# Kernel optimization log

Hardware: AMD Instinct MI355X
Metric: run time of the kernel (lower is better)

Reference implementation:

```python
import jax, jax.numpy as jnp
import numpy as np
import math

# e3nn-style fully-connected Clebsch-Gordan tensor product
# irreps_in1 = 64x0e + 64x1e + 64x2e   (dim 576)
# irreps_in2 =  1x0e +  1x1e +  1x2e   (dim 9, e.g. spherical harmonics)
# irreps_out = 64x0e + 64x1e + 64x2e   (dim 576), shared weights
MUL1, MUL2, MULO = 64, 1, 64
LS = [0, 1, 2]
N_BATCH = 32768


def _su2_cg(j1, m1, j2, m2, j3, m3):
    # SU(2) Clebsch-Gordan coefficient <j1 m1 j2 m2 | j3 m3> (Racah formula)
    if m3 != m1 + m2:
        return 0.0
    f = math.factorial
    c = (2 * j3 + 1) * f(j1 + j2 - j3) * f(j1 - j2 + j3) * f(-j1 + j2 + j3) / f(j1 + j2 + j3 + 1)
    c = math.sqrt(c)
    c *= math.sqrt(f(j3 + m3) * f(j3 - m3) * f(j1 - m1) * f(j1 + m1) * f(j2 - m2) * f(j2 + m2))
    s = 0.0
    for k in range(max(0, j2 - j3 - m1, j1 - j3 + m2), min(j1 + j2 - j3, j1 - m1, j2 + m2) + 1):
        s += (-1.0) ** k / (f(k) * f(j1 + j2 - j3 - k) * f(j1 - m1 - k) * f(j2 + m2 - k)
                            * f(j3 - j2 + m1 + k) * f(j3 - j1 - m2 + k))
    return c * s


def _q_real_to_complex(l):
    # unitary change of basis, columns = real-SH index, rows = complex m (e3nn convention)
    q = np.zeros((2 * l + 1, 2 * l + 1), dtype=np.complex128)
    r2 = 1.0 / math.sqrt(2.0)
    for m in range(-l, 0):
        q[l + m, l + abs(m)] = r2
        q[l + m, l - abs(m)] = -1j * r2
    q[l, l] = 1.0
    for m in range(1, l + 1):
        q[l + m, l + m] = (-1) ** m * r2
        q[l + m, l - m] = 1j * (-1) ** m * r2
    return (-1j) ** l * q


def _real_cg(l1, l2, l3):
    # CG tensor in the real spherical-harmonic basis, unit Frobenius norm (wigner_3j-like)
    C = np.zeros((2 * l1 + 1, 2 * l2 + 1, 2 * l3 + 1), dtype=np.complex128)
    for m1 in range(-l1, l1 + 1):
        for m2 in range(-l2, l2 + 1):
            m3 = m1 + m2
            if abs(m3) <= l3:
                C[l1 + m1, l2 + m2, l3 + m3] = _su2_cg(l1, m1, l2, m2, l3, m3)
    U1, U2, U3 = _q_real_to_complex(l1), _q_real_to_complex(l2), _q_real_to_complex(l3)
    Cr = np.einsum('ia,jb,kc,ijk->abc', U1, U2, np.conj(U3), C)
    assert np.abs(Cr.imag).max() < 1e-9, 'real-basis CG should be real'
    Cr = Cr.real
    return (Cr / np.linalg.norm(Cr)).astype(np.float32)


PATHS = [(l1, l2, l3) for l1 in LS for l2 in LS for l3 in LS if abs(l1 - l2) <= l3 <= l1 + l2]
CG = {p: jnp.asarray(_real_cg(*p)) for p in PATHS}
N_PATHS_TO = {l3: sum(1 for p in PATHS if p[2] == l3) for l3 in LS}
ALPHA = {l3: 1.0 / math.sqrt(MUL1 * MUL2 * N_PATHS_TO[l3]) for l3 in LS}  # path normalization
WEIGHT_NUMEL = len(PATHS) * MUL1 * MUL2 * MULO  # 15 * 4096 = 61440
DIM1 = MUL1 * sum(2 * l + 1 for l in LS)  # 576
DIM2 = MUL2 * sum(2 * l + 1 for l in LS)  # 9


def _split1(x):
    segs, off = [], 0
    for l in LS:
        d = MUL1 * (2 * l + 1)
        segs.append(x[:, off:off + d].reshape(-1, MUL1, 2 * l + 1))
        off += d
    return segs


def _split2(y):
    segs, off = [], 0
    for l in LS:
        d = 2 * l + 1
        segs.append(y[:, off:off + d])
        off += d
    return segs


def tensor_product(x, y, W):
    # W (x (CG-otimes) y): per-path weighted Clebsch-Gordan contraction
    xs, ys = _split1(x), _split2(y)  # xs[l]: [N,64,2l+1], ys[l]: [N,2l+1]
    N = x.shape[0]
    outs = [jnp.zeros((N, MULO, 2 * l + 1), x.dtype) for l in LS]
    off = 0
    for (l1, l2, l3) in PATHS:
        Wp = W[off:off + MUL1 * MULO].reshape(MUL1, MULO)  # [u, w] (v = 1)
        off += MUL1 * MULO
        outs[l3] = outs[l3] + ALPHA[l3] * jnp.einsum(
            'nui,nj,ijk,uw->nwk', xs[l1], ys[l2], CG[(l1, l2, l3)], Wp)
    return jnp.concatenate([o.reshape(N, -1) for o in outs], axis=-1)  # [N, 576]


def setup_inputs() -> dict:
    key = jax.random.key(0)
    kx, ky, kw = jax.random.split(key, 3)
    x = jax.random.normal(kx, (N_BATCH, DIM1), dtype=jnp.float32)
    y = jax.random.normal(ky, (N_BATCH, DIM2), dtype=jnp.float32)
    W = jax.random.normal(kw, (WEIGHT_NUMEL,), dtype=jnp.float32)
    return {'x': x, 'y': y, 'W': W}


def reference(x, y, W):
    return tensor_product(x, y, W)
```

## Files before the change

kernel.cpp:

```cpp
#include <hip/hip_runtime.h>
#include <cmath>
#include <complex>
#include <algorithm>

#define NPATH 15
constexpr int PL1[NPATH] = {0,0,0, 1,1,1,1,1,1, 2,2,2,2,2,2};
constexpr int PL2[NPATH] = {0,1,2, 0,1,1,1,2,2, 0,1,1,2,2,2};
constexpr int PL3[NPATH] = {0,1,2, 1,0,1,2,1,2, 2,1,2,0,1,2};
constexpr int CGOFF[NPATH] = {0,1,10,35,44,53,80,125,170,245,270,315,390,415,490};
constexpr int CGTOT = 615;
constexpr int YOFF[3] = {0,1,4};

constexpr int GB[8] = {0,9,24,33,48,63,88,103};
constexpr int YGTOT = 137;

struct CGArg { float v[CGTOT]; };

static double factd(int n){ double r=1.0; for(int i=2;i<=n;++i) r*=(double)i; return r; }

static double su2_cg(int j1,int m1,int j2,int m2,int j3,int m3){
  if (m3 != m1+m2) return 0.0;
  double c = (double)(2*j3+1) * factd(j1+j2-j3) * factd(j1-j2+j3) * factd(-j1+j2+j3)
             / factd(j1+j2+j3+1);
  c = std::sqrt(c);
  c *= std::sqrt(factd(j3+m3)*factd(j3-m3)*factd(j1-m1)*factd(j1+m1)*factd(j2-m2)*factd(j2+m2));
  double s = 0.0;
  int kmin = std::max(0, std::max(j2-j3-m1, j1-j3+m2));
  int kmax = std::min(j1+j2-j3, std::min(j1-m1, j2+m2));
  for (int k=kmin;k<=kmax;++k){
    double d = factd(k)*factd(j1+j2-j3-k)*factd(j1-m1-k)*factd(j2+m2-k)
             * factd(j3-j2+m1+k)*factd(j3-j1-m2+k);
    s += ((k&1)? -1.0 : 1.0)/d;
  }
  return c*s;
}

static void qmat(int l, std::complex<double>* q){
  int d = 2*l+1;
  for (int a=0;a<d*d;++a) q[a] = std::complex<double>(0.0,0.0);
  const double r2 = 1.0/std::sqrt(2.0);
  for (int m=-l; m<0; ++m){
    q[(l+m)*d + (l-m)] = std::complex<double>(r2, 0.0);
    q[(l+m)*d + (l+m)] = std::complex<double>(0.0, -r2);
  }
  q[l*d + l] = std::complex<double>(1.0,0.0);
  for (int m=1; m<=l; ++m){
    double sg = (m&1)? -1.0 : 1.0;
    q[(l+m)*d + (l+m)] = std::complex<double>(sg*r2, 0.0);
    q[(l+m)*d + (l-m)] = std::complex<double>(0.0, sg*r2);
  }
  std::complex<double> ph = (l==0)? std::complex<double>(1,0)
                        : (l==1)? std::complex<double>(0,-1)
                                : std::complex<double>(-1,0);
  for (int a=0;a<d*d;++a) q[a] *= ph;
}

static void compute_cg(float* outv){
  const int npaths_to[3] = {3,6,6};
  for (int p=0;p<NPATH;++p){
    int l1=PL1[p], l2=PL2[p], l3=PL3[p];
    int d1=2*l1+1, d2=2*l2+1, d3=2*l3+1;
    std::complex<double> C[5][5][5];
    for (int a=0;a<5;++a) for(int b=0;b<5;++b) for(int c=0;c<5;++c) C[a][b][c]=std::complex<double>(0,0);
    for (int m1=-l1;m1<=l1;++m1) for (int m2=-l2;m2<=l2;++m2){
      int m3=m1+m2;
      if (std::abs(m3)<=l3) C[l1+m1][l2+m2][l3+m3] = su2_cg(l1,m1,l2,m2,l3,m3);
    }
    std::complex<double> U1[25],U2[25],U3[25];
    qmat(l1,U1); qmat(l2,U2); qmat(l3,U3);
    double Cr[5][5][5]; double nrm=0.0;
    for (int a=0;a<d1;++a) for (int b=0;b<d2;++b) for (int c=0;c<d3;++c){
      std::complex<double> s(0,0);
      for (int i=0;i<d1;++i) for (int j=0;j<d2;++j) for (int k=0;k<d3;++k)
        s += U1[i*d1+a]*U2[j*d2+b]*std::conj(U3[k*d3+c])*C[i][j][k];
      Cr[a][b][c] = s.real();
      nrm += s.real()*s.real();
    }
    nrm = std::sqrt(nrm);
    double alpha = 1.0/std::sqrt(64.0*(double)npaths_to[l3]);
    float* o = outv + CGOFF[p];
    int idx=0;
    for (int a=0;a<d1;++a) for (int b=0;b<d2;++b) for (int c=0;c<d3;++c)
      o[idx++] = (float)(Cr[a][b][c]/nrm*alpha);
  }
}

typedef short bf16x8 __attribute__((ext_vector_type(8)));
typedef float f32x4 __attribute__((ext_vector_type(4)));

#define MFMA16(A,B,C) __builtin_amdgcn_mfma_f32_16x16x32_bf16((A),(B),(C),0,0,0)

__device__ __forceinline__ unsigned cvtpk_bf16(float a, float b){
  unsigned r;
  asm("v_cvt_pk_bf16_f32 %0, %1, %2" : "=v"(r) : "v"(a), "v"(b));
  return r;
}

__device__ __forceinline__ bf16x8 afrag(const unsigned short* s_xt, int plane, int kt, int row, int q){
  int c = (kt*4 + q) ^ (row & 7);
  return *reinterpret_cast<const bf16x8*>(s_xt + (plane*16 + row)*64 + c*8);
}
__device__ __forceinline__ bf16x8 wfrag(const unsigned short* WT, int p, int wt, int cl, int kt, int q){
  return *reinterpret_cast<const bf16x8*>(WT + p*4096 + (wt*16+cl)*64 + kt*32 + q*8);
}
__device__ __forceinline__ void xt_write_pk(unsigned short* s_xt, int plane, int n, int t16, uint2 pk){
  const int swz = (((t16>>1)^(n&7))<<3) + ((t16&1)<<2);
  *reinterpret_cast<uint2*>(s_xt + (plane*16 + n)*64 + swz) = pk;
}

__device__ __forceinline__ void pack_x(const float4& r0, const float4* r1, const float4* r2, uint2* xpk){
  const float* f0 = reinterpret_cast<const float*>(&r0);
  const float* f1 = reinterpret_cast<const float*>(r1);
  const float* f2 = reinterpret_cast<const float*>(r2);
  xpk[0].x = cvtpk_bf16(f0[0], f0[1]);  xpk[0].y = cvtpk_bf16(f0[2], f0[3]);
  #pragma unroll
  for (int i=0;i<3;++i){
    xpk[1+i].x = cvtpk_bf16(f1[0*3+i], f1[1*3+i]);
    xpk[1+i].y = cvtpk_bf16(f1[2*3+i], f1[3*3+i]);
  }
  #pragma unroll
  for (int i=0;i<5;++i){
    xpk[4+i].x = cvtpk_bf16(f2[0*5+i], f2[1*5+i]);
    xpk[4+i].y = cvtpk_bf16(f2[2*5+i], f2[3*5+i]);
  }
}

template<int G,int PB,int D1,int D3,int AB>
__device__ __forceinline__ void gen1(const unsigned short* s_xt, bf16x8 b0, bf16x8 b1,
                                     const float* yg4, f32x4* acc, int cl, int q){
  const f32x4 z4 = {0.f,0.f,0.f,0.f};
  #pragma unroll
  for (int i=0;i<D1;++i){
    bf16x8 a0 = afrag(s_xt, PB+i, 0, cl, q);
    bf16x8 a1 = afrag(s_xt, PB+i, 1, cl, q);
    f32x4 T = MFMA16(a0, b0, z4);  T = MFMA16(a1, b1, T);
    #pragma unroll
    for (int k=0;k<D3;++k){
      f32x4 yv = *reinterpret_cast<const f32x4*>(yg4 + (GB[G] + i*D3 + k)*16);
      acc[AB+k] += T*yv;
    }
  }
}
template<int PB,int D1,int AB>
__device__ __forceinline__ void dl0(const unsigned short* s_xt, bf16x8 b0, bf16x8 b1,
                                    f32x4 cy, f32x4* acc, int cl, int q){
  const f32x4 z4 = {0.f,0.f,0.f,0.f};
  #pragma unroll
  for (int i=0;i<D1;++i){
    bf16x8 a0 = afrag(s_xt, PB+i, 0, cl, q);
    bf16x8 a1 = afrag(s_xt, PB+i, 1, cl, q);
    f32x4 T = MFMA16(a0, b0, z4);  T = MFMA16(a1, b1, T);
    acc[AB+i] += cy*T;
  }
}
template<int D3,int YE,int AB>
__device__ __forceinline__ void d0l(const unsigned short* s_xt, bf16x8 b0, bf16x8 b1,
                                    float c, const float* yg4, f32x4* acc, int cl, int q){
  const f32x4 z4 = {0.f,0.f,0.f,0.f};
  bf16x8 a0 = afrag(s_xt, 0, 0, cl, q);
  bf16x8 a1 = afrag(s_xt, 0, 1, cl, q);
  f32x4 T = MFMA16(a0, b0, z4);  T = MFMA16(a1, b1, T);
  #pragma unroll
  for (int k=0;k<D3;++k){
    f32x4 yv = *reinterpret_cast<const f32x4*>(yg4 + (YE+k)*16);
    acc[AB+k] += (c*yv)*T;
  }
}
template<int PB,int D1,int YE>
__device__ __forceinline__ void dll0(const unsigned short* s_xt, bf16x8 b0, bf16x8 b1,
                                     float c, const float* yg4, f32x4* acc, int cl, int q){
  const f32x4 z4 = {0.f,0.f,0.f,0.f};
  f32x4 s = z4;
  #pragma unroll
  for (int i=0;i<D1;++i){
    bf16x8 a0 = afrag(s_xt, PB+i, 0, cl, q);
    bf16x8 a1 = afrag(s_xt, PB+i, 1, cl, q);
    f32x4 T = MFMA16(a0, b0, z4);  T = MFMA16(a1, b1, T);
    f32x4 yv = *reinterpret_cast<const f32x4*>(yg4 + (YE+i)*16);
    s += yv*T;
  }
  acc[0] += s*c;
}

__global__ __launch_bounds__(256, 4)
void tp_kernel(const float* __restrict__ x, const float* __restrict__ y,
               const unsigned short* __restrict__ WT, float* __restrict__ out, CGArg cga)
{
  __shared__ __align__(16) unsigned short s_xt[9*16*64];
  __shared__ __align__(16) float s_yg[YGTOT*16];

  const int bid = blockIdx.x;
  const int tile = (bid & 7) | ((bid >> 4) << 3);
  const int half = (bid >> 3) & 1;
  const int n0 = tile * 16;

  const int tid = threadIdx.x;
  const int n_s = tid>>4, t16 = tid&15;

  {
    const float* xb = x + (size_t)(n0 + n_s)*576;
    float4 r0 = *reinterpret_cast<const float4*>(xb + t16*4);
    float4 r1[3], r2[5];
    #pragma unroll
    for (int i=0;i<3;++i) r1[i] = *reinterpret_cast<const float4*>(xb + 64 + t16*12 + 4*i);
    #pragma unroll
    for (int i=0;i<5;++i) r2[i] = *reinterpret_cast<const float4*>(xb + 256 + t16*20 + 4*i);

    float yl[9];
    {
      const float* yrow = y + (size_t)(n0 + t16)*9;
      #pragma unroll
      for (int j=0;j<9;++j) yl[j] = yrow[j];
    }

    uint2 xpk[9];
    pack_x(r0, r1, r2, xpk);
    #pragma unroll
    for (int pl=0; pl<9; ++pl) xt_write_pk(s_xt, pl, n_s, t16, xpk[pl]);

    if (tid < 16){
      #pragma unroll
      for (int j=0;j<9;++j) s_yg[(128+j)*16 + tid] = yl[j];
    }

    if (half == 0){
      constexpr int GL[4] = {0,2,4,6};
      #pragma unroll
      for (int u=0; u<4; ++u){
        constexpr int GPp[4] = {5,7,10,13};
        const int p = GPp[u];
        const int d2=2*PL2[p]+1, d3=2*PL3[p]+1;
        const int cnt = (2*PL1[p]+1)*d3*16;
        for (int idx=tid; idx<cnt; idx+=256){
          int ik = idx >> 4;
          int i  = ik/d3;
          int k  = ik - i*d3;
          float s=0.f;
          for (int j=0;j<d2;++j)
            s += yl[YOFF[PL2[p]]+j]*cga.v[CGOFF[p]+(i*d2+j)*d3+k];
          s_yg[(GB[GL[u]]+ik)*16 + t16] = s;
        }
      }
    } else {
      constexpr int GL[4] = {1,3,5,7};
      #pragma unroll
      for (int u=0; u<4; ++u){
        constexpr int GPp[4] = {6,8,11,14};
        const int p = GPp[u];
        const int d2=2*PL2[p]+1, d3=2*PL3[p]+1;
        const int cnt = (2*PL1[p]+1)*d3*16;
        for (int idx=tid; idx<cnt; idx+=256){
          int ik = idx >> 4;
          int i  = ik/d3;
          int k  = ik - i*d3;
          float s=0.f;
          for (int j=0;j<d2;++j)
            s += yl[YOFF[PL2[p]]+j]*cga.v[CGOFF[p]+(i*d2+j)*d3+k];
          s_yg[(GB[GL[u]]+ik)*16 + t16] = s;
        }
      }
    }
  }
  __syncthreads();

  const int lane = tid & 63, wt = tid >> 6;
  const int cl = lane & 15, q = lane >> 4;
  const float* yg4 = s_yg + q*4;
  #define YV(E) (*reinterpret_cast<const f32x4*>(yg4 + (E)*16))

  const f32x4 z4 = {0.f,0.f,0.f,0.f};
  bf16x8 b0,b1,nb0,nb1;
  const f32x4 y0v = YV(128);
  const int wc = wt*16 + cl;

  #define LDB(P) { nb0 = wfrag(WT,P,wt,cl,0,q); nb1 = wfrag(WT,P,wt,cl,1,q); }
  #define ADV    { b0 = nb0; b1 = nb1; }

  if (half == 0){
    f32x4 acc[4] = {z4,z4,z4,z4};
    b0 = wfrag(WT,0,wt,cl,0,q); b1 = wfrag(WT,0,wt,cl,1,q);
    LDB(1);  dl0<0,1,0>(s_xt,b0,b1, cga.v[CGOFF[0]]*y0v, acc, cl,q);            ADV;
    LDB(3);  d0l<3,129,1>(s_xt,b0,b1, cga.v[CGOFF[1]], yg4, acc, cl,q);         ADV;
    LDB(4);  dl0<1,3,1>(s_xt,b0,b1, cga.v[CGOFF[3]]*y0v, acc, cl,q);            ADV;
    LDB(5);  dll0<1,3,129>(s_xt,b0,b1, cga.v[CGOFF[4]], yg4, acc, cl,q);        ADV;
    LDB(7);  gen1<0,1,3,3,1>(s_xt,b0,b1, yg4, acc, cl,q);                       ADV;
    LDB(10); gen1<2,1,3,3,1>(s_xt,b0,b1, yg4, acc, cl,q);                       ADV;
    LDB(12); gen1<4,4,5,3,1>(s_xt,b0,b1, yg4, acc, cl,q);                       ADV;
    LDB(13); dll0<4,5,132>(s_xt,b0,b1, cga.v[CGOFF[12]], yg4, acc, cl,q);       ADV;
             gen1<6,4,5,3,1>(s_xt,b0,b1, yg4, acc, cl,q);
    #pragma unroll
    for (int r=0;r<4;++r){
      float* orow = out + (size_t)(n0 + q*4 + r)*576;
      orow[wc] = acc[0][r];
      #pragma unroll
      for (int k=0;k<3;++k) orow[64 + wc*3 + k] = acc[1+k][r];
    }
  } else {
    f32x4 acc[5] = {z4,z4,z4,z4,z4};
    b0 = wfrag(WT,2,wt,cl,0,q); b1 = wfrag(WT,2,wt,cl,1,q);
    LDB(6);  d0l<5,132,0>(s_xt,b0,b1, cga.v[CGOFF[2]], yg4, acc, cl,q);         ADV;
    LDB(8);  gen1<1,1,3,5,0>(s_xt,b0,b1, yg4, acc, cl,q);                       ADV;
    LDB(9);  gen1<3,1,3,5,0>(s_xt,b0,b1, yg4, acc, cl,q);                       ADV;
    LDB(11); dl0<4,5,0>(s_xt,b0,b1, cga.v[CGOFF[9]]*y0v, acc, cl,q);            ADV;
    LDB(14); gen1<5,4,5,5,0>(s_xt,b0,b1, yg4, acc, cl,q);                       ADV;
             gen1<7,4,5,5,0>(s_xt,b0,b1, yg4, acc, cl,q);
    #pragma unroll
    for (int r=0;r<4;++r){
      float* orow = out + (size_t)(n0 + q*4 + r)*576;
      #pragma unroll
      for (int k=0;k<5;++k) orow[256 + wc*5 + k] = acc[k][r];
    }
  }
  #undef LDB
  #undef ADV
  #undef YV
}

__global__ void wt_kernel(const float* __restrict__ W, unsigned short* __restrict__ WT){
  int t = blockIdx.x*256 + threadIdx.x;
  int p = t >> 12, r = t & 4095, w = r >> 6, u = r & 63;
  float f = W[(p<<12) + (u<<6) + w];
  unsigned fu = __builtin_bit_cast(unsigned, f);
  unsigned rr = (fu + 0x7FFFu + ((fu>>16)&1u)) >> 16;
  WT[t] = (unsigned short)rr;
}

extern "C" void kernel_launch(void* const* d_in, const int* in_sizes, int n_in,
                              void* d_out, int out_size, void* d_ws, size_t ws_size,
                              hipStream_t stream) {
  const float* x = (const float*)d_in[0];
  const float* y = (const float*)d_in[1];
  const float* W = (const float*)d_in[2];
  float* out = (float*)d_out;
  (void)in_sizes; (void)n_in; (void)out_size; (void)ws_size;

  unsigned short* WT = (unsigned short*)d_ws;

  CGArg cga;
  compute_cg(cga.v);

  hipLaunchKernelGGL(wt_kernel, dim3(240), dim3(256), 0, stream, W, WT);
  hipLaunchKernelGGL(tp_kernel, dim3(4096), dim3(256), 0, stream, x, y, WT, out, cga);
}
```

Baseline: 57.25 us.

## Swap MFMA operand roles to hoist x fragments and vectorize output stores

Swaps the A/B operands of the MFMA so the accumulator layout becomes row = batch lane, column = 4 consecutive output channels. This lets each lane write contiguous float4 chunks of the interleaved output instead of scalar strided stores. The x fragments for each l1 block are now loaded from shared memory once and reused across paths rather than reloaded per path. The y-CG scalars become per-lane scalars rather than f32x4 vectors. The held x fragments (up to 18 bf16x8 registers) raise register pressure, which could hurt occupancy under the 256x4 launch bounds.

```diff
diff --git a/kernel.cpp b/kernel.cpp
--- a/kernel.cpp
+++ b/kernel.cpp
@@ -125,59 +125,50 @@
   }
 }
 
-template<int G,int PB,int D1,int D3,int AB>
-__device__ __forceinline__ void gen1(const unsigned short* s_xt, bf16x8 b0, bf16x8 b1,
-                                     const float* yg4, f32x4* acc, int cl, int q){
+template<int G,int D1,int D3,int AB>
+__device__ __forceinline__ void gen1(const bf16x8* xf, bf16x8 b0, bf16x8 b1,
+                                     const float* ygc, f32x4* acc){
   const f32x4 z4 = {0.f,0.f,0.f,0.f};
   #pragma unroll
   for (int i=0;i<D1;++i){
-    bf16x8 a0 = afrag(s_xt, PB+i, 0, cl, q);
-    bf16x8 a1 = afrag(s_xt, PB+i, 1, cl, q);
-    f32x4 T = MFMA16(a0, b0, z4);  T = MFMA16(a1, b1, T);
+    f32x4 T = MFMA16(b0, xf[2*i], z4);  T = MFMA16(b1, xf[2*i+1], T);
     #pragma unroll
     for (int k=0;k<D3;++k){
-      f32x4 yv = *reinterpret_cast<const f32x4*>(yg4 + (GB[G] + i*D3 + k)*16);
+      float yv = ygc[(GB[G] + i*D3 + k)*16];
       acc[AB+k] += T*yv;
     }
   }
 }
-template<int PB,int D1,int AB>
-__device__ __forceinline__ void dl0(const unsigned short* s_xt, bf16x8 b0, bf16x8 b1,
-                                    f32x4 cy, f32x4* acc, int cl, int q){
+template<int D1,int AB>
+__device__ __forceinline__ void dl0(const bf16x8* xf, bf16x8 b0, bf16x8 b1,
+                                    float cy, f32x4* acc){
   const f32x4 z4 = {0.f,0.f,0.f,0.f};
   #pragma unroll
   for (int i=0;i<D1;++i){
-    bf16x8 a0 = afrag(s_xt, PB+i, 0, cl, q);
-    bf16x8 a1 = afrag(s_xt, PB+i, 1, cl, q);
-    f32x4 T = MFMA16(a0, b0, z4);  T = MFMA16(a1, b1, T);
-    acc[AB+i] += cy*T;
+    f32x4 T = MFMA16(b0, xf[2*i], z4);  T = MFMA16(b1, xf[2*i+1], T);
+    acc[AB+i] += T*cy;
   }
 }
 template<int D3,int YE,int AB>
-__device__ __forceinline__ void d0l(const unsigned short* s_xt, bf16x8 b0, bf16x8 b1,
-                                    float c, const float* yg4, f32x4* acc, int cl, int q){
-  const f32x4 z4 = {0.f,0.f,0.f,0.f};
-  bf16x8 a0 = afrag(s_xt, 0, 0, cl, q);
-  bf16x8 a1 = afrag(s_xt, 0, 1, cl, q);
-  f32x4 T = MFMA16(a0, b0, z4);  T = MFMA16(a1, b1, T);
+__device__ __forceinline__ void d0l(const bf16x8* xf, bf16x8 b0, bf16x8 b1,
+                                    float c, const float* ygc, f32x4* acc){
+  const f32x4 z4 = {0.f,0.f,0.f,0.f};
+  f32x4 T = MFMA16(b0, xf[0], z4);  T = MFMA16(b1, xf[1], T);
   #pragma unroll
   for (int k=0;k<D3;++k){
-    f32x4 yv = *reinterpret_cast<const f32x4*>(yg4 + (YE+k)*16);
-    acc[AB+k] += (c*yv)*T;
-  }
-}
-template<int PB,int D1,int YE>
-__device__ __forceinline__ void dll0(const unsigned short* s_xt, bf16x8 b0, bf16x8 b1,
-                                     float c, const float* yg4, f32x4* acc, int cl, int q){
+    float yv = c*ygc[(YE+k)*16];
+    acc[AB+k] += T*yv;
+  }
+}
+template<int D1,int YE>
+__device__ __forceinline__ void dll0(const bf16x8* xf, bf16x8 b0, bf16x8 b1,
+                                     float c, const float* ygc, f32x4* acc){
   const f32x4 z4 = {0.f,0.f,0.f,0.f};
   f32x4 s = z4;
   #pragma unroll
   for (int i=0;i<D1;++i){
-    bf16x8 a0 = afrag(s_xt, PB+i, 0, cl, q);
-    bf16x8 a1 = afrag(s_xt, PB+i, 1, cl, q);
-    f32x4 T = MFMA16(a0, b0, z4);  T = MFMA16(a1, b1, T);
-    f32x4 yv = *reinterpret_cast<const f32x4*>(yg4 + (YE+i)*16);
-    s += yv*T;
+    f32x4 T = MFMA16(b0, xf[2*i], z4);  T = MFMA16(b1, xf[2*i+1], T);
+    s += T*ygc[(YE+i)*16];
   }
   acc[0] += s*c;
 }
@@ -265,55 +256,86 @@
 
   const int lane = tid & 63, wt = tid >> 6;
   const int cl = lane & 15, q = lane >> 4;
-  const float* yg4 = s_yg + q*4;
-  #define YV(E) (*reinterpret_cast<const f32x4*>(yg4 + (E)*16))
+  const float* ygc = s_yg + cl;
+  const float y0 = ygc[128*16];
+  const int wbase = wt*16 + q*4;
 
   const f32x4 z4 = {0.f,0.f,0.f,0.f};
   bf16x8 b0,b1,nb0,nb1;
-  const f32x4 y0v = YV(128);
-  const int wc = wt*16 + cl;
 
   #define LDB(P) { nb0 = wfrag(WT,P,wt,cl,0,q); nb1 = wfrag(WT,P,wt,cl,1,q); }
   #define ADV    { b0 = nb0; b1 = nb1; }
 
   if (half == 0){
     f32x4 acc[4] = {z4,z4,z4,z4};
+    bf16x8 xf0[2];
+    #pragma unroll
+    for (int kt=0;kt<2;++kt) xf0[kt] = afrag(s_xt, 0, kt, cl, q);
     b0 = wfrag(WT,0,wt,cl,0,q); b1 = wfrag(WT,0,wt,cl,1,q);
-    LDB(1);  dl0<0,1,0>(s_xt,b0,b1, cga.v[CGOFF[0]]*y0v, acc, cl,q);            ADV;
-    LDB(3);  d0l<3,129,1>(s_xt,b0,b1, cga.v[CGOFF[1]], yg4, acc, cl,q);         ADV;
-    LDB(4);  dl0<1,3,1>(s_xt,b0,b1, cga.v[CGOFF[3]]*y0v, acc, cl,q);            ADV;
-    LDB(5);  dll0<1,3,129>(s_xt,b0,b1, cga.v[CGOFF[4]], yg4, acc, cl,q);        ADV;
-    LDB(7);  gen1<0,1,3,3,1>(s_xt,b0,b1, yg4, acc, cl,q);                       ADV;
-    LDB(10); gen1<2,1,3,3,1>(s_xt,b0,b1, yg4, acc, cl,q);                       ADV;
-    LDB(12); gen1<4,4,5,3,1>(s_xt,b0,b1, yg4, acc, cl,q);                       ADV;
-    LDB(13); dll0<4,5,132>(s_xt,b0,b1, cga.v[CGOFF[12]], yg4, acc, cl,q);       ADV;
-             gen1<6,4,5,3,1>(s_xt,b0,b1, yg4, acc, cl,q);
-    #pragma unroll
-    for (int r=0;r<4;++r){
-      float* orow = out + (size_t)(n0 + q*4 + r)*576;
-      orow[wc] = acc[0][r];
-      #pragma unroll
-      for (int k=0;k<3;++k) orow[64 + wc*3 + k] = acc[1+k][r];
-    }
+
+    LDB(1);  dl0<1,0>(xf0, b0,b1, cga.v[CGOFF[0]]*y0, acc);              ADV;
+    LDB(3);  d0l<3,129,1>(xf0, b0,b1, cga.v[CGOFF[1]], ygc, acc);        ADV;
+    bf16x8 xf1[6];
+    #pragma unroll
+    for (int i=0;i<3;++i)
+      #pragma unroll
+      for (int kt=0;kt<2;++kt) xf1[2*i+kt] = afrag(s_xt, 1+i, kt, cl, q);
+    LDB(4);  dl0<3,1>(xf1, b0,b1, cga.v[CGOFF[3]]*y0, acc);              ADV;
+    LDB(5);  dll0<3,129>(xf1, b0,b1, cga.v[CGOFF[4]], ygc, acc);         ADV;
+    LDB(7);  gen1<0,3,3,1>(xf1, b0,b1, ygc, acc);                        ADV;
+    LDB(10); gen1<2,3,3,1>(xf1, b0,b1, ygc, acc);                        ADV;
+    bf16x8 xf2[10];
+    #pragma unroll
+    for (int i=0;i<5;++i)
+      #pragma unroll
+      for (int kt=0;kt<2;++kt) xf2[2*i+kt] = afrag(s_xt, 4+i, kt, cl, q);
+    LDB(12); gen1<4,5,3,1>(xf2, b0,b1, ygc, acc);                        ADV;
+    LDB(13); dll0<5,132>(xf2, b0,b1, cga.v[CGOFF[12]], ygc, acc);        ADV;
+             gen1<6,5,3,1>(xf2, b0,b1, ygc, acc);
+
+    float* orow = out + (size_t)(n0 + cl)*576;
+    *reinterpret_cast<float4*>(orow + wbase) =
+        make_float4(acc[0][0],acc[0][1],acc[0][2],acc[0][3]);
+    float4 v0 = make_float4(acc[1][0],acc[2][0],acc[3][0],acc[1][1]);
+    float4 v1 = make_float4(acc[2][1],acc[3][1],acc[1][2],acc[2][2]);
+    float4 v2 = make_float4(acc[3][2],acc[1][3],acc[2][3],acc[3][3]);
+    float4* qp = reinterpret_cast<float4*>(orow + 64 + wbase*3);
+    qp[0]=v0; qp[1]=v1; qp[2]=v2;
   } else {
     f32x4 acc[5] = {z4,z4,z4,z4,z4};
+    bf16x8 xf0[2];
+    #pragma unroll
+    for (int kt=0;kt<2;++kt) xf0[kt] = afrag(s_xt, 0, kt, cl, q);
     b0 = wfrag(WT,2,wt,cl,0,q); b1 = wfrag(WT,2,wt,cl,1,q);
-    LDB(6);  d0l<5,132,0>(s_xt,b0,b1, cga.v[CGOFF[2]], yg4, acc, cl,q);         ADV;
-    LDB(8);  gen1<1,1,3,5,0>(s_xt,b0,b1, yg4, acc, cl,q);                       ADV;
-    LDB(9);  gen1<3,1,3,5,0>(s_xt,b0,b1, yg4, acc, cl,q);                       ADV;
-    LDB(11); dl0<4,5,0>(s_xt,b0,b1, cga.v[CGOFF[9]]*y0v, acc, cl,q);            ADV;
-    LDB(14); gen1<5,4,5,5,0>(s_xt,b0,b1, yg4, acc, cl,q);                       ADV;
-             gen1<7,4,5,5,0>(s_xt,b0,b1, yg4, acc, cl,q);
-    #pragma unroll
-    for (int r=0;r<4;++r){
-      float* orow = out + (size_t)(n0 + q*4 + r)*576;
-      #pragma unroll
-      for (int k=0;k<5;++k) orow[256 + wc*5 + k] = acc[k][r];
-    }
+
+    LDB(6);  d0l<5,132,0>(xf0, b0,b1, cga.v[CGOFF[2]], ygc, acc);        ADV;
+    bf16x8 xf1[6];
+    #pragma unroll
+    for (int i=0;i<3;++i)
+      #pragma unroll
+      for (int kt=0;kt<2;++kt) xf1[2*i+kt] = afrag(s_xt, 1+i, kt, cl, q);
+    LDB(8);  gen1<1,3,5,0>(xf1, b0,b1, ygc, acc);                        ADV;
+    LDB(9);  gen1<3,3,5,0>(xf1, b0,b1, ygc, acc);                        ADV;
+    bf16x8 xf2[10];
+    #pragma unroll
+    for (int i=0;i<5;++i)
+      #pragma unroll
+      for (int kt=0;kt<2;++kt) xf2[2*i+kt] = afrag(s_xt, 4+i, kt, cl, q);
+    LDB(11); dl0<5,0>(xf2, b0,b1, cga.v[CGOFF[9]]*y0, acc);              ADV;
+    LDB(14); gen1<5,5,5,0>(xf2, b0,b1, ygc, acc);                        ADV;
+             gen1<7,5,5,0>(xf2, b0,b1, ygc, acc);
+
+    float* orow = out + (size_t)(n0 + cl)*576;
+    float4 v0 = make_float4(acc[0][0],acc[1][0],acc[2][0],acc[3][0]);
+    float4 v1 = make_float4(acc[4][0],acc[0][1],acc[1][1],acc[2][1]);
+    float4 v2 = make_float4(acc[3][1],acc[4][1],acc[0][2],acc[1][2]);
+    float4 v3 = make_float4(acc[2][2],acc[3][2],acc[4][2],acc[0][3]);
+    float4 v4 = make_float4(acc[1][3],acc[2][3],acc[3][3],acc[4][3]);
+    float4* qp = reinterpret_cast<float4*>(orow + 256 + wbase*5);
+    qp[0]=v0; qp[1]=v1; qp[2]=v2; qp[3]=v3; qp[4]=v4;
   }
   #undef LDB
   #undef ADV
-  #undef YV
 }
 
 __global__ void wt_kernel(const float* __restrict__ W, unsigned short* __restrict__ WT){
```

New measurement: 70.20 us. 22.6% more time.

## Process two 16-row tiles per block, swap MFMA operands for vectorized stores

Applied to the files above, without the earlier changes.

Each block now stages and computes two 16-row batch tiles, so every weight fragment loaded from global memory is reused across both tiles, and the grid is halved. The MFMA operand order is swapped so the accumulator layout puts batch rows along lanes, which lets the output be written as contiguous float4 stores instead of scattered scalar stores. The y-derived coefficient tables are compacted per half, and occupancy is lowered to 3 blocks per SM to make room for the doubled registers and shared memory. The cost is more register and LDS pressure and fewer resident waves to hide latency.

```diff
diff --git a/kernel.cpp b/kernel.cpp
--- a/kernel.cpp
+++ b/kernel.cpp
@@ -11,8 +11,7 @@
 constexpr int CGTOT = 615;
 constexpr int YOFF[3] = {0,1,4};
 
-constexpr int GB[8] = {0,9,24,33,48,63,88,103};
-constexpr int YGTOT = 137;
+constexpr int YGMAX = 89;
 
 struct CGArg { float v[CGTOT]; };
 
@@ -125,195 +124,241 @@
   }
 }
 
-template<int G,int PB,int D1,int D3,int AB>
-__device__ __forceinline__ void gen1(const unsigned short* s_xt, bf16x8 b0, bf16x8 b1,
-                                     const float* yg4, f32x4* acc, int cl, int q){
+template<int HALF>
+__device__ __forceinline__ void stage_tile(const float* __restrict__ x, const float* __restrict__ y,
+                                           int nbase, unsigned short* s_xt, float* s_yg,
+                                           const CGArg& cga, int tid, int n_s, int t16){
+  const float* xb = x + (size_t)(nbase + n_s)*576;
+  float4 r0 = *reinterpret_cast<const float4*>(xb + t16*4);
+  float4 r1[3], r2[5];
+  #pragma unroll
+  for (int i=0;i<3;++i) r1[i] = *reinterpret_cast<const float4*>(xb + 64 + t16*12 + 4*i);
+  #pragma unroll
+  for (int i=0;i<5;++i) r2[i] = *reinterpret_cast<const float4*>(xb + 256 + t16*20 + 4*i);
+
+  float yl[9];
+  {
+    const float* yrow = y + (size_t)(nbase + t16)*9;
+    #pragma unroll
+    for (int j=0;j<9;++j) yl[j] = yrow[j];
+  }
+
+  uint2 xpk[9];
+  pack_x(r0, r1, r2, xpk);
+  #pragma unroll
+  for (int pl=0; pl<9; ++pl) xt_write_pk(s_xt, pl, n_s, t16, xpk[pl]);
+
+  constexpr int RB = (HALF==0)? 48 : 80;
+  if (tid < 16){
+    #pragma unroll
+    for (int j=0;j<9;++j) s_yg[(RB+j)*16 + tid] = yl[j];
+  }
+
+  if constexpr (HALF==0){
+    constexpr int GPp[4] = {5,7,10,13};
+    constexpr int NB[4]  = {0,9,18,33};
+    #pragma unroll
+    for (int u=0; u<4; ++u){
+      const int p = GPp[u];
+      const int d2=2*PL2[p]+1, d3=2*PL3[p]+1;
+      const int cnt = (2*PL1[p]+1)*d3*16;
+      for (int idx=tid; idx<cnt; idx+=256){
+        int ik = idx >> 4;
+        int i  = ik/d3;
+        int k  = ik - i*d3;
+        float s=0.f;
+        for (int j=0;j<d2;++j)
+          s += yl[YOFF[PL2[p]]+j]*cga.v[CGOFF[p]+(i*d2+j)*d3+k];
+        s_yg[(NB[u]+ik)*16 + t16] = s;
+      }
+    }
+  } else {
+    constexpr int GPp[4] = {6,8,11,14};
+    constexpr int NB[4]  = {0,15,30,55};
+    #pragma unroll
+    for (int u=0; u<4; ++u){
+      const int p = GPp[u];
+      const int d2=2*PL2[p]+1, d3=2*PL3[p]+1;
+      const int cnt = (2*PL1[p]+1)*d3*16;
+      for (int idx=tid; idx<cnt; idx+=256){
+        int ik = idx >> 4;
+        int i  = ik/d3;
+        int k  = ik - i*d3;
+        float s=0.f;
+        for (int j=0;j<d2;++j)
+          s += yl[YOFF[PL2[p]]+j]*cga.v[CGOFF[p]+(i*d2+j)*d3+k];
+        s_yg[(NB[u]+ik)*16 + t16] = s;
+      }
+    }
+  }
+}
+
+template<int PB,int D1,int D3,int E0,int AB>
+__device__ __forceinline__ void gen2(const unsigned short* xt0, const unsigned short* xt1,
+                                     bf16x8 b0, bf16x8 b1,
+                                     const float* yg0, const float* yg1,
+                                     f32x4* a0, f32x4* a1, int cl, int q){
   const f32x4 z4 = {0.f,0.f,0.f,0.f};
   #pragma unroll
   for (int i=0;i<D1;++i){
-    bf16x8 a0 = afrag(s_xt, PB+i, 0, cl, q);
-    bf16x8 a1 = afrag(s_xt, PB+i, 1, cl, q);
-    f32x4 T = MFMA16(a0, b0, z4);  T = MFMA16(a1, b1, T);
+    f32x4 T0 = MFMA16(b0, afrag(xt0,PB+i,0,cl,q), z4);
+    T0       = MFMA16(b1, afrag(xt0,PB+i,1,cl,q), T0);
+    f32x4 T1 = MFMA16(b0, afrag(xt1,PB+i,0,cl,q), z4);
+    T1       = MFMA16(b1, afrag(xt1,PB+i,1,cl,q), T1);
     #pragma unroll
     for (int k=0;k<D3;++k){
-      f32x4 yv = *reinterpret_cast<const f32x4*>(yg4 + (GB[G] + i*D3 + k)*16);
-      acc[AB+k] += T*yv;
+      a0[AB+k] += T0*yg0[(E0+i*D3+k)*16];
+      a1[AB+k] += T1*yg1[(E0+i*D3+k)*16];
     }
   }
 }
 template<int PB,int D1,int AB>
-__device__ __forceinline__ void dl0(const unsigned short* s_xt, bf16x8 b0, bf16x8 b1,
-                                    f32x4 cy, f32x4* acc, int cl, int q){
+__device__ __forceinline__ void dl0_2(const unsigned short* xt0, const unsigned short* xt1,
+                                      bf16x8 b0, bf16x8 b1, float cy0, float cy1,
+                                      f32x4* a0, f32x4* a1, int cl, int q){
   const f32x4 z4 = {0.f,0.f,0.f,0.f};
   #pragma unroll
   for (int i=0;i<D1;++i){
-    bf16x8 a0 = afrag(s_xt, PB+i, 0, cl, q);
-    bf16x8 a1 = afrag(s_xt, PB+i, 1, cl, q);
-    f32x4 T = MFMA16(a0, b0, z4);  T = MFMA16(a1, b1, T);
-    acc[AB+i] += cy*T;
+    f32x4 T0 = MFMA16(b0, afrag(xt0,PB+i,0,cl,q), z4);
+    T0       = MFMA16(b1, afrag(xt0,PB+i,1,cl,q), T0);
+    f32x4 T1 = MFMA16(b0, afrag(xt1,PB+i,0,cl,q), z4);
+    T1       = MFMA16(b1, afrag(xt1,PB+i,1,cl,q), T1);
+    a0[AB+i] += T0*cy0;
+    a1[AB+i] += T1*cy1;
   }
 }
 template<int D3,int YE,int AB>
-__device__ __forceinline__ void d0l(const unsigned short* s_xt, bf16x8 b0, bf16x8 b1,
-                                    float c, const float* yg4, f32x4* acc, int cl, int q){
-  const f32x4 z4 = {0.f,0.f,0.f,0.f};
-  bf16x8 a0 = afrag(s_xt, 0, 0, cl, q);
-  bf16x8 a1 = afrag(s_xt, 0, 1, cl, q);
-  f32x4 T = MFMA16(a0, b0, z4);  T = MFMA16(a1, b1, T);
+__device__ __forceinline__ void d0l_2(const unsigned short* xt0, const unsigned short* xt1,
+                                      bf16x8 b0, bf16x8 b1, float c,
+                                      const float* yg0, const float* yg1,
+                                      f32x4* a0, f32x4* a1, int cl, int q){
+  const f32x4 z4 = {0.f,0.f,0.f,0.f};
+  f32x4 T0 = MFMA16(b0, afrag(xt0,0,0,cl,q), z4);
+  T0       = MFMA16(b1, afrag(xt0,0,1,cl,q), T0);
+  f32x4 T1 = MFMA16(b0, afrag(xt1,0,0,cl,q), z4);
+  T1       = MFMA16(b1, afrag(xt1,0,1,cl,q), T1);
   #pragma unroll
   for (int k=0;k<D3;++k){
-    f32x4 yv = *reinterpret_cast<const f32x4*>(yg4 + (YE+k)*16);
-    acc[AB+k] += (c*yv)*T;
+    a0[AB+k] += T0*(c*yg0[(YE+k)*16]);
+    a1[AB+k] += T1*(c*yg1[(YE+k)*16]);
   }
 }
 template<int PB,int D1,int YE>
-__device__ __forceinline__ void dll0(const unsigned short* s_xt, bf16x8 b0, bf16x8 b1,
-                                     float c, const float* yg4, f32x4* acc, int cl, int q){
-  const f32x4 z4 = {0.f,0.f,0.f,0.f};
-  f32x4 s = z4;
+__device__ __forceinline__ void dll0_2(const unsigned short* xt0, const unsigned short* xt1,
+                                       bf16x8 b0, bf16x8 b1, float c,
+                                       const float* yg0, const float* yg1,
+                                       f32x4* a0, f32x4* a1, int cl, int q){
+  const f32x4 z4 = {0.f,0.f,0.f,0.f};
+  f32x4 s0 = z4, s1 = z4;
   #pragma unroll
   for (int i=0;i<D1;++i){
-    bf16x8 a0 = afrag(s_xt, PB+i, 0, cl, q);
-    bf16x8 a1 = afrag(s_xt, PB+i, 1, cl, q);
-    f32x4 T = MFMA16(a0, b0, z4);  T = MFMA16(a1, b1, T);
-    f32x4 yv = *reinterpret_cast<const f32x4*>(yg4 + (YE+i)*16);
-    s += yv*T;
-  }
-  acc[0] += s*c;
-}
-
-__global__ __launch_bounds__(256, 4)
+    f32x4 T0 = MFMA16(b0, afrag(xt0,PB+i,0,cl,q), z4);
+    T0       = MFMA16(b1, afrag(xt0,PB+i,1,cl,q), T0);
+    f32x4 T1 = MFMA16(b0, afrag(xt1,PB+i,0,cl,q), z4);
+    T1       = MFMA16(b1, afrag(xt1,PB+i,1,cl,q), T1);
+    s0 += T0*yg0[(YE+i)*16];
+    s1 += T1*yg1[(YE+i)*16];
+  }
+  a0[0] += s0*c;
+  a1[0] += s1*c;
+}
+
+__global__ __launch_bounds__(256, 3)
 void tp_kernel(const float* __restrict__ x, const float* __restrict__ y,
                const unsigned short* __restrict__ WT, float* __restrict__ out, CGArg cga)
 {
-  __shared__ __align__(16) unsigned short s_xt[9*16*64];
-  __shared__ __align__(16) float s_yg[YGTOT*16];
+  __shared__ __align__(16) unsigned short s_xt0[9*16*64];
+  __shared__ __align__(16) unsigned short s_xt1[9*16*64];
+  __shared__ __align__(16) float s_yg0[YGMAX*16];
+  __shared__ __align__(16) float s_yg1[YGMAX*16];
 
   const int bid = blockIdx.x;
-  const int tile = (bid & 7) | ((bid >> 4) << 3);
+  const int pair = (bid & 7) | ((bid >> 4) << 3);
   const int half = (bid >> 3) & 1;
-  const int n0 = tile * 16;
+  const int n0 = pair * 32;
 
   const int tid = threadIdx.x;
   const int n_s = tid>>4, t16 = tid&15;
 
-  {
-    const float* xb = x + (size_t)(n0 + n_s)*576;
-    float4 r0 = *reinterpret_cast<const float4*>(xb + t16*4);
-    float4 r1[3], r2[5];
-    #pragma unroll
-    for (int i=0;i<3;++i) r1[i] = *reinterpret_cast<const float4*>(xb + 64 + t16*12 + 4*i);
-    #pragma unroll
-    for (int i=0;i<5;++i) r2[i] = *reinterpret_cast<const float4*>(xb + 256 + t16*20 + 4*i);
-
-    float yl[9];
-    {
-      const float* yrow = y + (size_t)(n0 + t16)*9;
-      #pragma unroll
-      for (int j=0;j<9;++j) yl[j] = yrow[j];
-    }
-
-    uint2 xpk[9];
-    pack_x(r0, r1, r2, xpk);
-    #pragma unroll
-    for (int pl=0; pl<9; ++pl) xt_write_pk(s_xt, pl, n_s, t16, xpk[pl]);
-
-    if (tid < 16){
-      #pragma unroll
-      for (int j=0;j<9;++j) s_yg[(128+j)*16 + tid] = yl[j];
-    }
-
-    if (half == 0){
-      constexpr int GL[4] = {0,2,4,6};
-      #pragma unroll
-      for (int u=0; u<4; ++u){
-        constexpr int GPp[4] = {5,7,10,13};
-        const int p = GPp[u];
-        const int d2=2*PL2[p]+1, d3=2*PL3[p]+1;
-        const int cnt = (2*PL1[p]+1)*d3*16;
-        for (int idx=tid; idx<cnt; idx+=256){
-          int ik = idx >> 4;
-          int i  = ik/d3;
-          int k  = ik - i*d3;
-          float s=0.f;
-          for (int j=0;j<d2;++j)
-            s += yl[YOFF[PL2[p]]+j]*cga.v[CGOFF[p]+(i*d2+j)*d3+k];
-          s_yg[(GB[GL[u]]+ik)*16 + t16] = s;
-        }
-      }
-    } else {
-      constexpr int GL[4] = {1,3,5,7};
-      #pragma unroll
-      for (int u=0; u<4; ++u){
-        constexpr int GPp[4] = {6,8,11,14};
-        const int p = GPp[u];
-        const int d2=2*PL2[p]+1, d3=2*PL3[p]+1;
-        const int cnt = (2*PL1[p]+1)*d3*16;
-        for (int idx=tid; idx<cnt; idx+=256){
-          int ik = idx >> 4;
-          int i  = ik/d3;
-          int k  = ik - i*d3;
-          float s=0.f;
-          for (int j=0;j<d2;++j)
-            s += yl[YOFF[PL2[p]]+j]*cga.v[CGOFF[p]+(i*d2+j)*d3+k];
-          s_yg[(GB[GL[u]]+ik)*16 + t16] = s;
-        }
-      }
-    }
+  if (half == 0){
+    stage_tile<0>(x, y, n0,    s_xt0, s_yg0, cga, tid, n_s, t16);
+    stage_tile<0>(x, y, n0+16, s_xt1, s_yg1, cga, tid, n_s, t16);
+  } else {
+    stage_tile<1>(x, y, n0,    s_xt0, s_yg0, cga, tid, n_s, t16);
+    stage_tile<1>(x, y, n0+16, s_xt1, s_yg1, cga, tid, n_s, t16);
   }
   __syncthreads();
 
   const int lane = tid & 63, wt = tid >> 6;
   const int cl = lane & 15, q = lane >> 4;
-  const float* yg4 = s_yg + q*4;
-  #define YV(E) (*reinterpret_cast<const f32x4*>(yg4 + (E)*16))
+  const float* yg0 = s_yg0 + cl;
+  const float* yg1 = s_yg1 + cl;
+  const int wbase = wt*16 + q*4;
 
   const f32x4 z4 = {0.f,0.f,0.f,0.f};
   bf16x8 b0,b1,nb0,nb1;
-  const f32x4 y0v = YV(128);
-  const int wc = wt*16 + cl;
 
   #define LDB(P) { nb0 = wfrag(WT,P,wt,cl,0,q); nb1 = wfrag(WT,P,wt,cl,1,q); }
   #define ADV    { b0 = nb0; b1 = nb1; }
 
   if (half == 0){
-    f32x4 acc[4] = {z4,z4,z4,z4};
+    constexpr int RB = 48;
+    const float y00 = yg0[RB*16], y01 = yg1[RB*16];
+    f32x4 a0[4] = {z4,z4,z4,z4};
+    f32x4 a1[4] = {z4,z4,z4,z4};
     b0 = wfrag(WT,0,wt,cl,0,q); b1 = wfrag(WT,0,wt,cl,1,q);
-    LDB(1);  dl0<0,1,0>(s_xt,b0,b1, cga.v[CGOFF[0]]*y0v, acc, cl,q);            ADV;
-    LDB(3);  d0l<3,129,1>(s_xt,b0,b1, cga.v[CGOFF[1]], yg4, acc, cl,q);         ADV;
-    LDB(4);  dl0<1,3,1>(s_xt,b0,b1, cga.v[CGOFF[3]]*y0v, acc, cl,q);            ADV;
-    LDB(5);  dll0<1,3,129>(s_xt,b0,b1, cga.v[CGOFF[4]], yg4, acc, cl,q);        ADV;
-    LDB(7);  gen1<0,1,3,3,1>(s_xt,b0,b1, yg4, acc, cl,q);                       ADV;
-    LDB(10); gen1<2,1,3,3,1>(s_xt,b0,b1, yg4, acc, cl,q);                       ADV;
-    LDB(12); gen1<4,4,5,3,1>(s_xt,b0,b1, yg4, acc, cl,q);                       ADV;
-    LDB(13); dll0<4,5,132>(s_xt,b0,b1, cga.v[CGOFF[12]], yg4, acc, cl,q);       ADV;
-             gen1<6,4,5,3,1>(s_xt,b0,b1, yg4, acc, cl,q);
-    #pragma unroll
-    for (int r=0;r<4;++r){
-      float* orow = out + (size_t)(n0 + q*4 + r)*576;
-      orow[wc] = acc[0][r];
-      #pragma unroll
-      for (int k=0;k<3;++k) orow[64 + wc*3 + k] = acc[1+k][r];
+
+    LDB(1);  dl0_2<0,1,0>(s_xt0,s_xt1, b0,b1, cga.v[CGOFF[0]]*y00, cga.v[CGOFF[0]]*y01, a0,a1, cl,q); ADV;
+    LDB(3);  d0l_2<3,RB+1,1>(s_xt0,s_xt1, b0,b1, cga.v[CGOFF[1]], yg0,yg1, a0,a1, cl,q);              ADV;
+    LDB(4);  dl0_2<1,3,1>(s_xt0,s_xt1, b0,b1, cga.v[CGOFF[3]]*y00, cga.v[CGOFF[3]]*y01, a0,a1, cl,q); ADV;
+    LDB(5);  dll0_2<1,3,RB+1>(s_xt0,s_xt1, b0,b1, cga.v[CGOFF[4]], yg0,yg1, a0,a1, cl,q);             ADV;
+    LDB(7);  gen2<1,3,3,0,1>(s_xt0,s_xt1, b0,b1, yg0,yg1, a0,a1, cl,q);                               ADV;
+    LDB(10); gen2<1,3,3,9,1>(s_xt0,s_xt1, b0,b1, yg0,yg1, a0,a1, cl,q);                               ADV;
+    LDB(12); gen2<4,5,3,18,1>(s_xt0,s_xt1, b0,b1, yg0,yg1, a0,a1, cl,q);                              ADV;
+    LDB(13); dll0_2<4,5,RB+4>(s_xt0,s_xt1, b0,b1, cga.v[CGOFF[12]], yg0,yg1, a0,a1, cl,q);            ADV;
+             gen2<4,5,3,33,1>(s_xt0,s_xt1, b0,b1, yg0,yg1, a0,a1, cl,q);
+
+    #pragma unroll
+    for (int tt=0; tt<2; ++tt){
+      const f32x4* a = (tt==0)? a0 : a1;
+      float* orow = out + (size_t)(n0 + tt*16 + cl)*576;
+      *reinterpret_cast<float4*>(orow + wbase) =
+          make_float4(a[0][0],a[0][1],a[0][2],a[0][3]);
+      float4 v0 = make_float4(a[1][0],a[2][0],a[3][0],a[1][1]);
+      float4 v1 = make_float4(a[2][1],a[3][1],a[1][2],a[2][2]);
+      float4 v2 = make_float4(a[3][2],a[1][3],a[2][3],a[3][3]);
+      float4* qp = reinterpret_cast<float4*>(orow + 64 + wbase*3);
+      qp[0]=v0; qp[1]=v1; qp[2]=v2;
     }
   } else {
-    f32x4 acc[5] = {z4,z4,z4,z4,z4};
+    constexpr int RB = 80;
+    const float y00 = yg0[RB*16], y01 = yg1[RB*16];
+    f32x4 a0[5] = {z4,z4,z4,z4,z4};
+    f32x4 a1[5] = {z4,z4,z4,z4,z4};
     b0 = wfrag(WT,2,wt,cl,0,q); b1 = wfrag(WT,2,wt,cl,1,q);
-    LDB(6);  d0l<5,132,0>(s_xt,b0,b1, cga.v[CGOFF[2]], yg4, acc, cl,q);         ADV;
-    LDB(8);  gen1<1,1,3,5,0>(s_xt,b0,b1, yg4, acc, cl,q);                       ADV;
-    LDB(9);  gen1<3,1,3,5,0>(s_xt,b0,b1, yg4, acc, cl,q);                       ADV;
-    LDB(11); dl0<4,5,0>(s_xt,b0,b1, cga.v[CGOFF[9]]*y0v, acc, cl,q);            ADV;
-    LDB(14); gen1<5,4,5,5,0>(s_xt,b0,b1, yg4, acc, cl,q);                       ADV;
-             gen1<7,4,5,5,0>(s_xt,b0,b1, yg4, acc, cl,q);
-    #pragma unroll
-    for (int r=0;r<4;++r){
-      float* orow = out + (size_t)(n0 + q*4 + r)*576;
-      #pragma unroll
-      for (int k=0;k<5;++k) orow[256 + wc*5 + k] = acc[k][r];
+
+    LDB(6);  d0l_2<5,RB+4,0>(s_xt0,s_xt1, b0,b1, cga.v[CGOFF[2]], yg0,yg1, a0,a1, cl,q);              ADV;
+    LDB(8);  gen2<1,3,5,0,0>(s_xt0,s_xt1, b0,b1, yg0,yg1, a0,a1, cl,q);                               ADV;
+    LDB(9);  gen2<1,3,5,15,0>(s_xt0,s_xt1, b0,b1, yg0,yg1, a0,a1, cl,q);                              ADV;
+    LDB(11); dl0_2<4,5,0>(s_xt0,s_xt1, b0,b1, cga.v[CGOFF[9]]*y00, cga.v[CGOFF[9]]*y01, a0,a1, cl,q); ADV;
+    LDB(14); gen2<4,5,5,30,0>(s_xt0,s_xt1, b0,b1, yg0,yg1, a0,a1, cl,q);                              ADV;
+             gen2<4,5,5,55,0>(s_xt0,s_xt1, b0,b1, yg0,yg1, a0,a1, cl,q);
+
+    #pragma unroll
+    for (int tt=0; tt<2; ++tt){
+      const f32x4* a = (tt==0)? a0 : a1;
+      float* orow = out + (size_t)(n0 + tt*16 + cl)*576;
+      float4 v0 = make_float4(a[0][0],a[1][0],a[2][0],a[3][0]);
+      float4 v1 = make_float4(a[4][0],a[0][1],a[1][1],a[2][1]);
+      float4 v2 = make_float4(a[3][1],a[4][1],a[0][2],a[1][2]);
+      float4 v3 = make_float4(a[2][2],a[3][2],a[4][2],a[0][3]);
+      float4 v4 = make_float4(a[1][3],a[2][3],a[3][3],a[4][3]);
+      float4* qp = reinterpret_cast<float4*>(orow + 256 + wbase*5);
+      qp[0]=v0; qp[1]=v1; qp[2]=v2; qp[3]=v3; qp[4]=v4;
     }
   }
   #undef LDB
   #undef ADV
-  #undef YV
 }
 
 __global__ void wt_kernel(const float* __restrict__ W, unsigned short* __restrict__ WT){
@@ -340,5 +385,5 @@
   compute_cg(cga.v);
 
   hipLaunchKernelGGL(wt_kernel, dim3(240), dim3(256), 0, stream, W, WT);
-  hipLaunchKernelGGL(tp_kernel, dim3(4096), dim3(256), 0, stream, x, y, WT, out, cga);
-}
+  hipLaunchKernelGGL(tp_kernel, dim3(2048), dim3(256), 0, stream, x, y, WT, out, cga);
+}
```

New measurement: 55.13 us, median of 2. -3.7%, faster.
